# Kernel optimization log

Hardware: AMD Instinct MI355X
Metric: run time of the kernel (lower is better)

Reference implementation:

```python
import jax, jax.numpy as jnp
import numpy as np

H = 32  # hidden_size
T = 7   # num_day (seq_len)
F = 1   # num_feature
B = 262144


def _glorot(key, shape):
    # mimic torch uniform(-1/sqrt(H), 1/sqrt(H)) init for LSTM/Linear params
    bound = 1.0 / np.sqrt(H)
    return jax.random.uniform(key, shape, jnp.float32, -bound, bound)


def setup_inputs() -> dict:
    key = jax.random.key(0)
    ks = jax.random.split(key, 14)
    return {
        "inputs": jax.random.normal(ks[0], (B, T, F), jnp.float32),
        # layer 0 (input_size=F)
        "W_ih0": _glorot(ks[1], (4 * H, F)),
        "W_hh0": _glorot(ks[2], (4 * H, H)),
        "b_ih0": _glorot(ks[3], (4 * H,)),
        "b_hh0": _glorot(ks[4], (4 * H,)),
        # layer 1 (input_size=H)
        "W_ih1": _glorot(ks[5], (4 * H, H)),
        "W_hh1": _glorot(ks[6], (4 * H, H)),
        "b_ih1": _glorot(ks[7], (4 * H,)),
        "b_hh1": _glorot(ks[8], (4 * H,)),
        # fc: Linear(H, 1)
        "fc_w": _glorot(ks[9], (1, H)),
        "fc_b": _glorot(ks[10], (1,)),
        # fc1: Linear(T, 1)
        "fc1_w": jax.random.uniform(ks[11], (1, T), jnp.float32, -1.0 / np.sqrt(T), 1.0 / np.sqrt(T)),
        "fc1_b": jax.random.uniform(ks[12], (1,), jnp.float32, -1.0 / np.sqrt(T), 1.0 / np.sqrt(T)),
    }


def _lstm_layer(x_tbf, W_ih, W_hh, b):
    # x_tbf: [T, B, in]; PyTorch gate order: i, f, g, o
    Bdim = x_tbf.shape[1]
    h0 = jnp.zeros((Bdim, H), x_tbf.dtype)
    c0 = jnp.zeros((Bdim, H), x_tbf.dtype)

    def step(carry, x_t):
        h, c = carry
        gates = x_t @ W_ih.T + h @ W_hh.T + b  # [B, 4H]
        i, f, g, o = jnp.split(gates, 4, axis=-1)
        i = jax.nn.sigmoid(i)
        f = jax.nn.sigmoid(f)
        g = jnp.tanh(g)
        o = jax.nn.sigmoid(o)
        c = f * c + i * g
        h = o * jnp.tanh(c)
        return (h, c), h

    _, hs = jax.lax.scan(step, (h0, c0), x_tbf)
    return hs  # [T, B, H]


def reference(inputs, W_ih0, W_hh0, b_ih0, b_hh0, W_ih1, W_hh1, b_ih1, b_hh1,
              fc_w, fc_b, fc1_w, fc1_b):
    x = jnp.transpose(inputs, (1, 0, 2))            # [T, B, F]
    h1 = _lstm_layer(x, W_ih0, W_hh0, b_ih0 + b_hh0)  # [T, B, H]
    h2 = _lstm_layer(h1, W_ih1, W_hh1, b_ih1 + b_hh1)  # [T, B, H]
    out = jnp.transpose(h2, (1, 0, 2))              # [B, T, H]
    y = out @ fc_w.T + fc_b                          # [B, T, 1]
    y = jnp.squeeze(y, 2)                            # [B, T]
    y = y @ fc1_w.T + fc1_b                          # [B, 1]
    return y
```

## Files before the change

kernel.cpp:

```cpp
#include <hip/hip_runtime.h>


#define HID 32
#define TSTEPS 7
#define LSTRIDE 40
#define NWAVES 8

typedef _Float16 half8 __attribute__((ext_vector_type(8)));
typedef float floatx4 __attribute__((ext_vector_type(4)));
typedef float floatx2 __attribute__((ext_vector_type(2)));

#define LOG2E 1.44269504088896f

__device__ __forceinline__ float fast_rcp(float x) { return __builtin_amdgcn_rcpf(x); }

__device__ __forceinline__ float exp2_fast(float x) {
#if __has_builtin(__builtin_amdgcn_exp2f)
    return __builtin_amdgcn_exp2f(x);
#else
    return __expf(x * 0.69314718055994531f);
#endif
}

__device__ __forceinline__ float sigm_pre(float s) {
    return fast_rcp(1.0f + exp2_fast(s));
}
__device__ __forceinline__ float tanh_pre(float s) {
    return fmaf(-2.0f, fast_rcp(exp2_fast(s) + 1.0f), 1.0f);
}
__device__ __forceinline__ float tanh_raw(float x) {
    return tanh_pre(x * (2.0f * LOG2E));
}

__global__ __launch_bounds__(512, 6) void lstm2_mfma(
    const float* __restrict__ xin,
    const float* __restrict__ Wih0,
    const float* __restrict__ Whh0,
    const float* __restrict__ bih0,
    const float* __restrict__ bhh0,
    const float* __restrict__ Wih1,
    const float* __restrict__ Whh1,
    const float* __restrict__ bih1,
    const float* __restrict__ bhh1,
    const float* __restrict__ fcw,
    const float* __restrict__ fcb,
    const float* __restrict__ fc1w,
    const float* __restrict__ fc1b,
    float* __restrict__ out,
    int B)
{
    const int lane = threadIdx.x & 63;
    const int wave = threadIdx.x >> 6;
    const int col  = lane & 15;
    const int rg   = lane >> 4;
    const int seq_base = (blockIdx.x * NWAVES + wave) * 16;

    __shared__ __align__(16) _Float16 ldsw[3 * 8 * 64 * 8];
    __shared__ __align__(16) floatx2  ldsbw0[128];
    __shared__ float                  ldsb1[128];
    __shared__ __align__(16) _Float16 ldsh[NWAVES][2][16 * LSTRIDE];
    __shared__ __align__(16) float    ldsx[NWAVES][TSTEPS * 16];

    _Float16* h1l = &ldsh[wave][0][0];
    _Float16* h2l = &ldsh[wave][1][0];
    float* xl = &ldsx[wave][0];

#pragma unroll
    for (int e = lane; e < TSTEPS * 16; e += 64) {
        const int s = e / TSTEPS;
        const int tt = e - s * TSTEPS;
        xl[tt * 16 + s] = xin[seq_base * TSTEPS + e];
    }

    if (wave < 3) {
        const float* Wsrc = (wave == 0) ? Whh0 : (wave == 1) ? Wih1 : Whh1;
#pragma unroll
        for (int nt = 0; nt < 8; ++nt) {
            const int n = nt * 16 + col;
            const float sc = ((n >> 5) == 2) ? (2.0f * LOG2E) : (-LOG2E);
            const float* s = Wsrc + n * HID + rg * 8;
            half8 f;
#pragma unroll
            for (int j = 0; j < 8; ++j) f[j] = (_Float16)(sc * s[j]);
            *(half8*)&ldsw[((wave * 8 + nt) * 64 + lane) * 8] = f;
        }
    } else if (wave == 3) {
#pragma unroll
        for (int i = 0; i < 2; ++i) {
            const int n = i * 64 + lane;
            const float sc = ((n >> 5) == 2) ? (2.0f * LOG2E) : (-LOG2E);
            floatx2 bw;
            bw[0] = sc * (bih0[n] + bhh0[n]);
            bw[1] = sc * Wih0[n];
            ldsbw0[n] = bw;
            ldsb1[n]  = sc * (bih1[n] + bhh1[n]);
        }
    }
    __syncthreads();

    const float fcw_l0 = fcw[col];
    const float fcw_l1 = fcw[16 + col];

    half8 Ah1 = {};
    half8 Ah2 = {};
    float c1[2][4] = {}, c2[2][4] = {};
    float facc[4] = {0.f, 0.f, 0.f, 0.f};

    for (int t = 0; t < TSTEPS; ++t) {
        unsigned woff = 0;
        asm volatile("" : "+v"(woff));
        const char* wB  = (const char*)ldsw   + lane * 16 + woff;
        const char* bB0 = (const char*)ldsbw0 + col * 8  + woff;
        const char* bB1 = (const char*)ldsb1  + col * 4  + woff;

        const floatx4 xr = *(const floatx4*)&xl[t * 16 + rg * 4];

        floatx4 g0[8];
#pragma unroll
        for (int nt = 0; nt < 8; ++nt) {
            const floatx2 bw = *(const floatx2*)(bB0 + nt * 128);
            const half8 bf   = *(const half8*)(wB + nt * 1024);
            floatx4 c;
#pragma unroll
            for (int r = 0; r < 4; ++r) c[r] = fmaf(bw[1], xr[r], bw[0]);
            g0[nt] = __builtin_amdgcn_mfma_f32_16x16x32_f16(Ah1, bf, c, 0, 0, 0);
        }

#pragma unroll
        for (int q = 0; q < 2; ++q) {
#pragma unroll
            for (int r = 0; r < 4; ++r) {
                const float ii = sigm_pre(g0[0 + q][r]);
                const float ff = sigm_pre(g0[2 + q][r]);
                const float gg = tanh_pre(g0[4 + q][r]);
                const float oo = sigm_pre(g0[6 + q][r]);
                const float c  = ff * c1[q][r] + ii * gg;
                c1[q][r] = c;
                const float h = oo * tanh_raw(c);
                h1l[(rg * 4 + r) * LSTRIDE + q * 16 + col] = (_Float16)h;
            }
        }
        Ah1 = *(const half8*)&h1l[col * LSTRIDE + rg * 8];

        floatx4 g1[8];
#pragma unroll
        for (int nt = 0; nt < 8; ++nt) {
            const float b1  = *(const float*)(bB1 + nt * 64);
            const half8 f1a = *(const half8*)(wB + 8192  + nt * 1024);
            const half8 f1b = *(const half8*)(wB + 16384 + nt * 1024);
            floatx4 c = {b1, b1, b1, b1};
            c = __builtin_amdgcn_mfma_f32_16x16x32_f16(Ah1, f1a, c, 0, 0, 0);
            g1[nt] = __builtin_amdgcn_mfma_f32_16x16x32_f16(Ah2, f1b, c, 0, 0, 0);
        }

        const float f1t = fc1w[t];
        const float w0 = f1t * fcw_l0;
        const float w1 = f1t * fcw_l1;
#pragma unroll
        for (int q = 0; q < 2; ++q) {
            const float wq = q ? w1 : w0;
#pragma unroll
            for (int r = 0; r < 4; ++r) {
                const float ii = sigm_pre(g1[0 + q][r]);
                const float ff = sigm_pre(g1[2 + q][r]);
                const float gg = tanh_pre(g1[4 + q][r]);
                const float oo = sigm_pre(g1[6 + q][r]);
                const float c  = ff * c2[q][r] + ii * gg;
                c2[q][r] = c;
                const float h = oo * tanh_raw(c);
                facc[r] = fmaf(wq, h, facc[r]);
                h2l[(rg * 4 + r) * LSTRIDE + q * 16 + col] = (_Float16)h;
            }
        }
        Ah2 = *(const half8*)&h2l[col * LSTRIDE + rg * 8];
    }

#pragma unroll
    for (int r = 0; r < 4; ++r) {
        float v = facc[r];
        v += __shfl_xor(v, 1);
        v += __shfl_xor(v, 2);
        v += __shfl_xor(v, 4);
        v += __shfl_xor(v, 8);
        facc[r] = v;
    }
    float sum_f1 = 0.f;
#pragma unroll
    for (int t = 0; t < TSTEPS; ++t) sum_f1 += fc1w[t];
    const float tail = fcb[0] * sum_f1 + fc1b[0];

    if (col == 0) {
#pragma unroll
        for (int r = 0; r < 4; ++r)
            out[seq_base + rg * 4 + r] = facc[r] + tail;
    }
}

extern "C" void kernel_launch(void* const* d_in, const int* in_sizes, int n_in,
                              void* d_out, int out_size, void* d_ws, size_t ws_size,
                              hipStream_t stream) {
    const float* xin  = (const float*)d_in[0];
    const float* Wih0 = (const float*)d_in[1];
    const float* Whh0 = (const float*)d_in[2];
    const float* bih0 = (const float*)d_in[3];
    const float* bhh0 = (const float*)d_in[4];
    const float* Wih1 = (const float*)d_in[5];
    const float* Whh1 = (const float*)d_in[6];
    const float* bih1 = (const float*)d_in[7];
    const float* bhh1 = (const float*)d_in[8];
    const float* fcw  = (const float*)d_in[9];
    const float* fcb  = (const float*)d_in[10];
    const float* fc1w = (const float*)d_in[11];
    const float* fc1b = (const float*)d_in[12];
    float* out = (float*)d_out;

    const int B = in_sizes[0] / TSTEPS;
    const int grid = B / (NWAVES * 16);
    lstm2_mfma<<<grid, NWAVES * 64, 0, stream>>>(
        xin, Wih0, Whh0, bih0, bhh0, Wih1, Whh1, bih1, bhh1,
        fcw, fcb, fc1w, fc1b, out, B);
}
```

Measured before the change: 202.4 us.

## Merge gate reciprocals algebraically and double waves per block

New measurement: 199.4 us. About the same (-1.5%).

```diff
diff --git a/kernel.cpp b/kernel.cpp
--- a/kernel.cpp
+++ b/kernel.cpp
@@ -4,7 +4,7 @@
 #define HID 32
 #define TSTEPS 7
 #define LSTRIDE 40
-#define NWAVES 8
+#define NWAVES 16
 
 typedef _Float16 half8 __attribute__((ext_vector_type(8)));
 typedef float floatx4 __attribute__((ext_vector_type(4)));
@@ -22,17 +22,7 @@
 #endif
 }
 
-__device__ __forceinline__ float sigm_pre(float s) {
-    return fast_rcp(1.0f + exp2_fast(s));
-}
-__device__ __forceinline__ float tanh_pre(float s) {
-    return fmaf(-2.0f, fast_rcp(exp2_fast(s) + 1.0f), 1.0f);
-}
-__device__ __forceinline__ float tanh_raw(float x) {
-    return tanh_pre(x * (2.0f * LOG2E));
-}
-
-__global__ __launch_bounds__(512, 6) void lstm2_mfma(
+__global__ __launch_bounds__(1024, 8) void lstm2_mfma(
     const float* __restrict__ xin,
     const float* __restrict__ Wih0,
     const float* __restrict__ Whh0,
@@ -72,19 +62,22 @@
         xl[tt * 16 + s] = xin[seq_base * TSTEPS + e];
     }
 
-    if (wave < 3) {
-        const float* Wsrc = (wave == 0) ? Whh0 : (wave == 1) ? Wih1 : Whh1;
-#pragma unroll
-        for (int nt = 0; nt < 8; ++nt) {
+    if (wave < 6) {
+        const int m = wave >> 1;
+        const float* Wsrc = (m == 0) ? Whh0 : (m == 1) ? Wih1 : Whh1;
+        const int nt0 = (wave & 1) * 4;
+#pragma unroll
+        for (int k = 0; k < 4; ++k) {
+            const int nt = nt0 + k;
             const int n = nt * 16 + col;
             const float sc = ((n >> 5) == 2) ? (2.0f * LOG2E) : (-LOG2E);
             const float* s = Wsrc + n * HID + rg * 8;
             half8 f;
 #pragma unroll
             for (int j = 0; j < 8; ++j) f[j] = (_Float16)(sc * s[j]);
-            *(half8*)&ldsw[((wave * 8 + nt) * 64 + lane) * 8] = f;
-        }
-    } else if (wave == 3) {
+            *(half8*)&ldsw[((m * 8 + nt) * 64 + lane) * 8] = f;
+        }
+    } else if (wave == 6) {
 #pragma unroll
         for (int i = 0; i < 2; ++i) {
             const int n = i * 64 + lane;
@@ -129,15 +122,30 @@
 #pragma unroll
         for (int q = 0; q < 2; ++q) {
 #pragma unroll
-            for (int r = 0; r < 4; ++r) {
-                const float ii = sigm_pre(g0[0 + q][r]);
-                const float ff = sigm_pre(g0[2 + q][r]);
-                const float gg = tanh_pre(g0[4 + q][r]);
-                const float oo = sigm_pre(g0[6 + q][r]);
-                const float c  = ff * c1[q][r] + ii * gg;
-                c1[q][r] = c;
-                const float h = oo * tanh_raw(c);
-                h1l[(rg * 4 + r) * LSTRIDE + q * 16 + col] = (_Float16)h;
+            for (int rp = 0; rp < 2; ++rp) {
+                float Ea[2], Db[2], Ed[2], Ee[2];
+#pragma unroll
+                for (int e = 0; e < 2; ++e) {
+                    const int r = rp * 2 + e;
+                    Ea[e] = exp2_fast(g0[0 + q][r]);
+                    Db[e] = 1.0f + exp2_fast(g0[2 + q][r]);
+                    Ed[e] = exp2_fast(g0[4 + q][r]);
+                    Ee[e] = exp2_fast(g0[6 + q][r]);
+                }
+                const float Rb = fast_rcp(Db[0] * Db[1]);
+#pragma unroll
+                for (int e = 0; e < 2; ++e) {
+                    const int r = rp * 2 + e;
+                    const float ff  = Rb * Db[1 - e];
+                    const float Rig = fast_rcp((1.0f + Ea[e]) * (1.0f + Ed[e]));
+                    const float ig  = fmaf(Ed[e], Rig, -Rig);
+                    const float c   = fmaf(ff, c1[q][r], ig);
+                    c1[q][r] = c;
+                    const float Ec  = exp2_fast(c * (2.0f * LOG2E));
+                    const float Rh  = fast_rcp((1.0f + Ee[e]) * (1.0f + Ec));
+                    const float h   = fmaf(Ec, Rh, -Rh);
+                    h1l[(rg * 4 + r) * LSTRIDE + q * 16 + col] = (_Float16)h;
+                }
             }
         }
         Ah1 = *(const half8*)&h1l[col * LSTRIDE + rg * 8];
@@ -160,16 +168,31 @@
         for (int q = 0; q < 2; ++q) {
             const float wq = q ? w1 : w0;
 #pragma unroll
-            for (int r = 0; r < 4; ++r) {
-                const float ii = sigm_pre(g1[0 + q][r]);
-                const float ff = sigm_pre(g1[2 + q][r]);
-                const float gg = tanh_pre(g1[4 + q][r]);
-                const float oo = sigm_pre(g1[6 + q][r]);
-                const float c  = ff * c2[q][r] + ii * gg;
-                c2[q][r] = c;
-                const float h = oo * tanh_raw(c);
-                facc[r] = fmaf(wq, h, facc[r]);
-                h2l[(rg * 4 + r) * LSTRIDE + q * 16 + col] = (_Float16)h;
+            for (int rp = 0; rp < 2; ++rp) {
+                float Ea[2], Db[2], Ed[2], Ee[2];
+#pragma unroll
+                for (int e = 0; e < 2; ++e) {
+                    const int r = rp * 2 + e;
+                    Ea[e] = exp2_fast(g1[0 + q][r]);
+                    Db[e] = 1.0f + exp2_fast(g1[2 + q][r]);
+                    Ed[e] = exp2_fast(g1[4 + q][r]);
+                    Ee[e] = exp2_fast(g1[6 + q][r]);
+                }
+                const float Rb = fast_rcp(Db[0] * Db[1]);
+#pragma unroll
+                for (int e = 0; e < 2; ++e) {
+                    const int r = rp * 2 + e;
+                    const float ff  = Rb * Db[1 - e];
+                    const float Rig = fast_rcp((1.0f + Ea[e]) * (1.0f + Ed[e]));
+                    const float ig  = fmaf(Ed[e], Rig, -Rig);
+                    const float c   = fmaf(ff, c2[q][r], ig);
+                    c2[q][r] = c;
+                    const float Ec  = exp2_fast(c * (2.0f * LOG2E));
+                    const float Rh  = fast_rcp((1.0f + Ee[e]) * (1.0f + Ec));
+                    const float h   = fmaf(Ec, Rh, -Rh);
+                    facc[r] = fmaf(wq, h, facc[r]);
+                    h2l[(rg * 4 + r) * LSTRIDE + q * 16 + col] = (_Float16)h;
+                }
             }
         }
         Ah2 = *(const half8*)&h2l[col * LSTRIDE + rg * 8];
```
